# Optimization experiments

Hardware: AMD Instinct MI355X
Metric: run time of the kernel (lower is better)

Reference implementation:

```python
import jax, jax.numpy as jnp
import numpy as np

LATENT = 3
HIDDEN = 16
INP = LATENT + 1  # prev_z cat action
B = 1048576


def setup_inputs() -> dict:
    key = jax.random.key(0)
    ks = jax.random.split(key, 11)
    s_ih = 1.0 / np.sqrt(HIDDEN)
    return {
        "prev_z": jax.random.normal(ks[0], (B, LATENT), jnp.float32),
        "action": jax.random.normal(ks[1], (B, 1), jnp.float32),
        "prev_h": jax.random.normal(ks[2], (B, HIDDEN), jnp.float32),
        # GRUCell params (torch layout: [3*H, in] and [3*H, H], gate order r,z,n)
        "W_ih": jax.random.uniform(ks[3], (3 * HIDDEN, INP), jnp.float32, -s_ih, s_ih),
        "W_hh": jax.random.uniform(ks[4], (3 * HIDDEN, HIDDEN), jnp.float32, -s_ih, s_ih),
        "b_ih": jax.random.uniform(ks[5], (3 * HIDDEN,), jnp.float32, -s_ih, s_ih),
        "b_hh": jax.random.uniform(ks[6], (3 * HIDDEN,), jnp.float32, -s_ih, s_ih),
        # prior heads
        "W_mu": jax.random.uniform(ks[7], (LATENT, HIDDEN), jnp.float32, -s_ih, s_ih),
        "b_mu": jax.random.uniform(ks[8], (LATENT,), jnp.float32, -s_ih, s_ih),
        "W_lv": jax.random.uniform(ks[9], (LATENT, HIDDEN), jnp.float32, -s_ih, s_ih),
        "b_lv": jax.random.uniform(ks[10], (LATENT,), jnp.float32, -s_ih, s_ih),
    }


def reference(prev_z, action, prev_h, W_ih, W_hh, b_ih, b_hh, W_mu, b_mu, W_lv, b_lv):
    x = jnp.concatenate([prev_z, action], axis=-1)              # [B, 4]
    gi = x @ W_ih.T + b_ih                                       # [B, 3H]
    gh = prev_h @ W_hh.T + b_hh                                  # [B, 3H]
    i_r, i_z, i_n = jnp.split(gi, 3, axis=-1)
    h_r, h_z, h_n = jnp.split(gh, 3, axis=-1)
    r = jax.nn.sigmoid(i_r + h_r)
    z = jax.nn.sigmoid(i_z + h_z)
    n = jnp.tanh(i_n + r * h_n)
    h = (1.0 - z) * n + z * prev_h                               # [B, H]
    mu = h @ W_mu.T + b_mu                                       # [B, 3]
    logvar = jnp.clip(h @ W_lv.T + b_lv, -5.0, 5.0)              # [B, 3]
    return mu, logvar, h
```

## Files before the change

### kernel.cpp

```cpp
#include <hip/hip_runtime.h>

#define TPB 256
#define WPT 4

typedef _Float16 half8 __attribute__((ext_vector_type(8)));
typedef float f32x4 __attribute__((ext_vector_type(4)));

__device__ __forceinline__ float fast_sigmoid(float x) {
    return __builtin_amdgcn_rcpf(1.0f + __expf(-x));
}
__device__ __forceinline__ float fast_tanh(float x) {
    return 2.0f * __builtin_amdgcn_rcpf(1.0f + __expf(-2.0f * x)) - 1.0f;
}


__global__ __launch_bounds__(64) void prep_kernel(
    const float* __restrict__ W_ih, const float* __restrict__ W_hh,
    const float* __restrict__ b_ih, const float* __restrict__ b_hh,
    const float* __restrict__ W_mu, const float* __restrict__ b_mu,
    const float* __restrict__ W_lv, const float* __restrict__ b_lv,
    void* __restrict__ wsv)
{
    _Float16* wsB  = (_Float16*)wsv;
    _Float16* wsA2 = wsB + 2048;
    const int l = threadIdx.x;
    const int col = l & 15, kg = l >> 4;

    #pragma unroll
    for (int t = 0; t < 4; ++t) {
        const int gate = (t == 0) ? col : (t == 1) ? (16 + col) : (32 + col);
        #pragma unroll
        for (int i = 0; i < 8; ++i) {
            const int k = kg * 8 + i;
            float v = 0.f;
            if (t <= 1) {
                if (k < 4)       v = W_ih[gate * 4 + k];
                else if (k < 20) v = W_hh[gate * 16 + (k - 4)];
            } else if (t == 2) {
                if (k < 4)       v = W_ih[gate * 4 + k];
            } else {
                if (k >= 4 && k < 20) v = W_hh[gate * 16 + (k - 4)];
            }
            wsB[t * 512 + l * 8 + i] = (_Float16)v;
        }
    }
    #pragma unroll
    for (int i = 0; i < 8; ++i) {
        const int k = kg * 8 + i;
        const int m = col;
        float v = 0.f;
        if (m < 3) {
            if (k < 16)       v = W_mu[m * 16 + k];
            else if (k == 20) v = b_mu[m];
        } else if (m < 6) {
            if (k < 16)       v = W_lv[(m - 3) * 16 + k];
            else if (k == 20) v = b_lv[m - 3];
        }
        wsA2[l * 8 + i] = (_Float16)v;
    }
    if (l < 16) {
        float4* b4 = (float4*)((char*)wsv + 5120);
        b4[l] = make_float4(b_ih[l] + b_hh[l],
                            b_ih[16 + l] + b_hh[16 + l],
                            b_ih[32 + l],
                            b_hh[32 + l]);
    }
}

__global__ __launch_bounds__(TPB) void rssm_kernel(
    const float* __restrict__ prev_z,
    const float* __restrict__ action,
    const float* __restrict__ prev_h,
    const void*  __restrict__ wsv,
    float* __restrict__ out_mu,
    float* __restrict__ out_lv,
    float* __restrict__ out_h,
    int B)
{
    __shared__ float lds[4][WPT][16 * 20];
    const int tid  = threadIdx.x;
    const int wid  = tid >> 6, lane = tid & 63;
    const int col  = lane & 15, kg = lane >> 4;
    const int wbase = (blockIdx.x * 4 + wid) * (16 * WPT);
    if (wbase >= B) return;

    const _Float16* wsB  = (const _Float16*)wsv;
    const _Float16* wsA2 = wsB + 2048;
    const float4*   wsB4 = (const float4*)((const char*)wsv + 5120);

    const half8* Bp = (const half8*)wsB;
    const half8 bR  = Bp[lane];
    const half8 bZ  = Bp[64 + lane];
    const half8 bNi = Bp[128 + lane];
    const half8 bNh = Bp[192 + lane];
    const half8 a2  = ((const half8*)wsA2)[lane];
    const float4 bias = wsB4[col];

    half8 a[WPT];
    if (kg == 0) {
        #pragma unroll
        for (int t = 0; t < WPT; ++t) {
            const int arow = min(wbase + t * 16 + col, B - 1);
            const float z0 = prev_z[arow * 3 + 0];
            const float z1 = prev_z[arow * 3 + 1];
            const float z2 = prev_z[arow * 3 + 2];
            const float ac = action[arow];
            const float4 h03 = *(const float4*)(prev_h + (size_t)arow * 16);
            a[t][0] = (_Float16)z0;    a[t][1] = (_Float16)z1;
            a[t][2] = (_Float16)z2;    a[t][3] = (_Float16)ac;
            a[t][4] = (_Float16)h03.x; a[t][5] = (_Float16)h03.y;
            a[t][6] = (_Float16)h03.z; a[t][7] = (_Float16)h03.w;
        }
    } else if (kg == 1) {
        #pragma unroll
        for (int t = 0; t < WPT; ++t) {
            const int arow = min(wbase + t * 16 + col, B - 1);
            const float4 u = *(const float4*)(prev_h + (size_t)arow * 16 + 4);
            const float4 v = *(const float4*)(prev_h + (size_t)arow * 16 + 8);
            a[t][0] = (_Float16)u.x; a[t][1] = (_Float16)u.y;
            a[t][2] = (_Float16)u.z; a[t][3] = (_Float16)u.w;
            a[t][4] = (_Float16)v.x; a[t][5] = (_Float16)v.y;
            a[t][6] = (_Float16)v.z; a[t][7] = (_Float16)v.w;
        }
    } else if (kg == 2) {
        #pragma unroll
        for (int t = 0; t < WPT; ++t) {
            const int arow = min(wbase + t * 16 + col, B - 1);
            const float4 w = *(const float4*)(prev_h + (size_t)arow * 16 + 12);
            a[t][0] = (_Float16)w.x; a[t][1] = (_Float16)w.y;
            a[t][2] = (_Float16)w.z; a[t][3] = (_Float16)w.w;
            a[t][4] = (_Float16)0.f; a[t][5] = (_Float16)0.f;
            a[t][6] = (_Float16)0.f; a[t][7] = (_Float16)0.f;
        }
    } else {
        #pragma unroll
        for (int t = 0; t < WPT; ++t)
            #pragma unroll
            for (int i = 0; i < 8; ++i) a[t][i] = (_Float16)0.f;
    }

    float hp[WPT][4];
    #pragma unroll
    for (int t = 0; t < WPT; ++t) {
        const int rbase = wbase + t * 16 + kg * 4;
        #pragma unroll
        for (int q = 0; q < 4; ++q)
            hp[t][q] = prev_h[(size_t)min(rbase + q, B - 1) * 16 + col];
    }

    #pragma unroll
    for (int t = 0; t < WPT; ++t) {
        f32x4 accR  = {bias.x, bias.x, bias.x, bias.x};
        f32x4 accZ  = {bias.y, bias.y, bias.y, bias.y};
        f32x4 accNi = {bias.z, bias.z, bias.z, bias.z};
        f32x4 accNh = {bias.w, bias.w, bias.w, bias.w};
        accR  = __builtin_amdgcn_mfma_f32_16x16x32_f16(a[t], bR,  accR,  0, 0, 0);
        accZ  = __builtin_amdgcn_mfma_f32_16x16x32_f16(a[t], bZ,  accZ,  0, 0, 0);
        accNi = __builtin_amdgcn_mfma_f32_16x16x32_f16(a[t], bNi, accNi, 0, 0, 0);
        accNh = __builtin_amdgcn_mfma_f32_16x16x32_f16(a[t], bNh, accNh, 0, 0, 0);

        const int rbase = wbase + t * 16 + kg * 4;
        float* ldst = &lds[wid][t][0];
        #pragma unroll
        for (int q = 0; q < 4; ++q) {
            const float r  = fast_sigmoid(accR[q]);
            const float z  = fast_sigmoid(accZ[q]);
            const float n  = fast_tanh(fmaf(r, accNh[q], accNi[q]));
            const float hv = fmaf(z, hp[t][q] - n, n);
            const int rr = rbase + q;
            if (rr < B) out_h[(size_t)min(rr, B - 1) * 16 + col] = hv;
            ldst[(kg * 4 + q) * 20 + col] = hv;
        }
    }

    #pragma unroll
    for (int t = 0; t < WPT; ++t) {
        half8 b2;
        if (kg < 2) {
            const float4 p0 = *(const float4*)&lds[wid][t][col * 20 + kg * 8];
            const float4 p1 = *(const float4*)&lds[wid][t][col * 20 + kg * 8 + 4];
            b2[0] = (_Float16)p0.x; b2[1] = (_Float16)p0.y;
            b2[2] = (_Float16)p0.z; b2[3] = (_Float16)p0.w;
            b2[4] = (_Float16)p1.x; b2[5] = (_Float16)p1.y;
            b2[6] = (_Float16)p1.z; b2[7] = (_Float16)p1.w;
        } else if (kg == 2) {
            #pragma unroll
            for (int i = 0; i < 8; ++i) b2[i] = (_Float16)0.f;
            b2[4] = (_Float16)1.0f;
        } else {
            #pragma unroll
            for (int i = 0; i < 8; ++i) b2[i] = (_Float16)0.f;
        }

        f32x4 acc2 = {0.f, 0.f, 0.f, 0.f};
        acc2 = __builtin_amdgcn_mfma_f32_16x16x32_f16(a2, b2, acc2, 0, 0, 0);

        const int brow = wbase + t * 16 + col;
        if (brow < B) {
            if (kg == 0) {
                out_mu[brow * 3 + 0] = acc2[0];
                out_mu[brow * 3 + 1] = acc2[1];
                out_mu[brow * 3 + 2] = acc2[2];
                out_lv[brow * 3 + 0] = fminf(fmaxf(acc2[3], -5.0f), 5.0f);
            } else if (kg == 1) {
                out_lv[brow * 3 + 1] = fminf(fmaxf(acc2[0], -5.0f), 5.0f);
                out_lv[brow * 3 + 2] = fminf(fmaxf(acc2[1], -5.0f), 5.0f);
            }
        }
    }
}

extern "C" void kernel_launch(void* const* d_in, const int* in_sizes, int n_in,
                              void* d_out, int out_size, void* d_ws, size_t ws_size,
                              hipStream_t stream) {
    const float* prev_z = (const float*)d_in[0];
    const float* action = (const float*)d_in[1];
    const float* prev_h = (const float*)d_in[2];
    const float* W_ih   = (const float*)d_in[3];
    const float* W_hh   = (const float*)d_in[4];
    const float* b_ih   = (const float*)d_in[5];
    const float* b_hh   = (const float*)d_in[6];
    const float* W_mu   = (const float*)d_in[7];
    const float* b_mu   = (const float*)d_in[8];
    const float* W_lv   = (const float*)d_in[9];
    const float* b_lv   = (const float*)d_in[10];

    const int B = in_sizes[0] / 3;
    float* out    = (float*)d_out;
    float* out_mu = out;
    float* out_lv = out + (size_t)3 * B;
    float* out_h  = out + (size_t)6 * B;

    prep_kernel<<<1, 64, 0, stream>>>(W_ih, W_hh, b_ih, b_hh,
                                      W_mu, b_mu, W_lv, b_lv, d_ws);

    const int rows_per_block = 4 * 16 * WPT;
    const int blocks = (B + rows_per_block - 1) / rows_per_block;
    rssm_kernel<<<blocks, TPB, 0, stream>>>(prev_z, action, prev_h, d_ws,
                                            out_mu, out_lv, out_h, B);
}
```

Baseline: 51.74 us.

## Stage inputs and outputs through LDS for coalesced float4 global access

```diff
diff --git a/kernel.cpp b/kernel.cpp
--- a/kernel.cpp
+++ b/kernel.cpp
@@ -2,8 +2,13 @@
 
 #define TPB 256
 #define WPT 4
+#define ROW_DW 20
+#define LDS_ROW_F32 (64 * ROW_DW)
+#define LDS_MU_F32 192
+#define LDS_WAVE_F32 (LDS_ROW_F32 + 2 * LDS_MU_F32)
 
 typedef _Float16 half8 __attribute__((ext_vector_type(8)));
+typedef __fp16  fp16x2 __attribute__((ext_vector_type(2)));
 typedef float f32x4 __attribute__((ext_vector_type(4)));
 
 __device__ __forceinline__ float fast_sigmoid(float x) {
@@ -11,6 +16,14 @@
 }
 __device__ __forceinline__ float fast_tanh(float x) {
     return 2.0f * __builtin_amdgcn_rcpf(1.0f + __expf(-2.0f * x)) - 1.0f;
+}
+__device__ __forceinline__ half8 pack8(float4 lo, float4 hi) {
+    union { fp16x2 p[4]; half8 h; } u;
+    u.p[0] = __builtin_amdgcn_cvt_pkrtz(lo.x, lo.y);
+    u.p[1] = __builtin_amdgcn_cvt_pkrtz(lo.z, lo.w);
+    u.p[2] = __builtin_amdgcn_cvt_pkrtz(hi.x, hi.y);
+    u.p[3] = __builtin_amdgcn_cvt_pkrtz(hi.z, hi.w);
+    return u.h;
 }
 
 
@@ -21,8 +34,7 @@
     const float* __restrict__ W_lv, const float* __restrict__ b_lv,
     void* __restrict__ wsv)
 {
-    _Float16* wsB  = (_Float16*)wsv;
-    _Float16* wsA2 = wsB + 2048;
+    _Float16* wsB = (_Float16*)wsv;
     const int l = threadIdx.x;
     const int col = l & 15, kg = l >> 4;
 
@@ -47,6 +59,11 @@
     #pragma unroll
     for (int i = 0; i < 8; ++i) {
         const int k = kg * 8 + i;
+        wsB[4 * 512 + l * 8 + i] = (_Float16)((k == col + 4) ? 1.f : 0.f);
+    }
+    #pragma unroll
+    for (int i = 0; i < 8; ++i) {
+        const int k = kg * 8 + i;
         const int m = col;
         float v = 0.f;
         if (m < 3) {
@@ -56,10 +73,10 @@
             if (k < 16)       v = W_lv[(m - 3) * 16 + k];
             else if (k == 20) v = b_lv[m - 3];
         }
-        wsA2[l * 8 + i] = (_Float16)v;
+        wsB[5 * 512 + l * 8 + i] = (_Float16)v;
     }
     if (l < 16) {
-        float4* b4 = (float4*)((char*)wsv + 5120);
+        float4* b4 = (float4*)((char*)wsv + 6144);
         b4[l] = make_float4(b_ih[l] + b_hh[l],
                             b_ih[16 + l] + b_hh[16 + l],
                             b_ih[32 + l],
@@ -77,135 +94,109 @@
     float* __restrict__ out_h,
     int B)
 {
-    __shared__ float lds[4][WPT][16 * 20];
-    const int tid  = threadIdx.x;
-    const int wid  = tid >> 6, lane = tid & 63;
-    const int col  = lane & 15, kg = lane >> 4;
-    const int wbase = (blockIdx.x * 4 + wid) * (16 * WPT);
+    __shared__ float lds[4][LDS_WAVE_F32];
+    const int tid = threadIdx.x;
+    const int wid = tid >> 6, lane = tid & 63;
+    const int col = lane & 15, kg = lane >> 4;
+    const int wbase = (blockIdx.x * 4 + wid) * 64;
     if (wbase >= B) return;
 
-    const _Float16* wsB  = (const _Float16*)wsv;
-    const _Float16* wsA2 = wsB + 2048;
-    const float4*   wsB4 = (const float4*)((const char*)wsv + 5120);
-
-    const half8* Bp = (const half8*)wsB;
+    float* W  = lds[wid];
+    float* MU = W + LDS_ROW_F32;
+    float* LV = MU + LDS_MU_F32;
+
+    const half8* Bp = (const half8*)wsv;
     const half8 bR  = Bp[lane];
     const half8 bZ  = Bp[64 + lane];
     const half8 bNi = Bp[128 + lane];
     const half8 bNh = Bp[192 + lane];
-    const half8 a2  = ((const half8*)wsA2)[lane];
-    const float4 bias = wsB4[col];
-
-    half8 a[WPT];
-    if (kg == 0) {
+    const half8 bHp = Bp[256 + lane];
+    const half8 a2  = Bp[320 + lane];
+    const float4 bias = ((const float4*)((const char*)wsv + 6144))[col];
+
+    {
+        const float4* hg = (const float4*)prev_h;
         #pragma unroll
-        for (int t = 0; t < WPT; ++t) {
-            const int arow = min(wbase + t * 16 + col, B - 1);
-            const float z0 = prev_z[arow * 3 + 0];
-            const float z1 = prev_z[arow * 3 + 1];
-            const float z2 = prev_z[arow * 3 + 2];
-            const float ac = action[arow];
-            const float4 h03 = *(const float4*)(prev_h + (size_t)arow * 16);
-            a[t][0] = (_Float16)z0;    a[t][1] = (_Float16)z1;
-            a[t][2] = (_Float16)z2;    a[t][3] = (_Float16)ac;
-            a[t][4] = (_Float16)h03.x; a[t][5] = (_Float16)h03.y;
-            a[t][6] = (_Float16)h03.z; a[t][7] = (_Float16)h03.w;
-        }
-    } else if (kg == 1) {
-        #pragma unroll
-        for (int t = 0; t < WPT; ++t) {
-            const int arow = min(wbase + t * 16 + col, B - 1);
-            const float4 u = *(const float4*)(prev_h + (size_t)arow * 16 + 4);
-            const float4 v = *(const float4*)(prev_h + (size_t)arow * 16 + 8);
-            a[t][0] = (_Float16)u.x; a[t][1] = (_Float16)u.y;
-            a[t][2] = (_Float16)u.z; a[t][3] = (_Float16)u.w;
-            a[t][4] = (_Float16)v.x; a[t][5] = (_Float16)v.y;
-            a[t][6] = (_Float16)v.z; a[t][7] = (_Float16)v.w;
-        }
-    } else if (kg == 2) {
-        #pragma unroll
-        for (int t = 0; t < WPT; ++t) {
-            const int arow = min(wbase + t * 16 + col, B - 1);
-            const float4 w = *(const float4*)(prev_h + (size_t)arow * 16 + 12);
-            a[t][0] = (_Float16)w.x; a[t][1] = (_Float16)w.y;
-            a[t][2] = (_Float16)w.z; a[t][3] = (_Float16)w.w;
-            a[t][4] = (_Float16)0.f; a[t][5] = (_Float16)0.f;
-            a[t][6] = (_Float16)0.f; a[t][7] = (_Float16)0.f;
-        }
-    } else {
-        #pragma unroll
-        for (int t = 0; t < WPT; ++t)
-            #pragma unroll
-            for (int i = 0; i < 8; ++i) a[t][i] = (_Float16)0.f;
-    }
-
-    float hp[WPT][4];
+        for (int i = 0; i < 4; ++i) {
+            const int fi = i * 64 + lane;
+            const int r = fi >> 2, w = fi & 3;
+            const int gi = min(wbase * 4 + fi, B * 4 - 1);
+            const float4 v = hg[gi];
+            *(float4*)&W[r * ROW_DW + 4 + w * 4] = v;
+        }
+        const int zr = min(wbase + lane, B - 1);
+        const float z0 = prev_z[zr * 3 + 0];
+        const float z1 = prev_z[zr * 3 + 1];
+        const float z2 = prev_z[zr * 3 + 2];
+        const float ac = action[zr];
+        *(float4*)&W[lane * ROW_DW] = make_float4(z0, z1, z2, ac);
+    }
+
     #pragma unroll
     for (int t = 0; t < WPT; ++t) {
-        const int rbase = wbase + t * 16 + kg * 4;
-        #pragma unroll
-        for (int q = 0; q < 4; ++q)
-            hp[t][q] = prev_h[(size_t)min(rbase + q, B - 1) * 16 + col];
-    }
-
-    #pragma unroll
-    for (int t = 0; t < WPT; ++t) {
+        const float* ap = &W[(t * 16 + col) * ROW_DW + kg * 8];
+        const float4 z4 = make_float4(0.f, 0.f, 0.f, 0.f);
+        const float4 p0 = (kg < 3) ? *(const float4*)ap : z4;
+        const float4 p1 = (kg < 2) ? *(const float4*)(ap + 4) : z4;
+        const half8 a = pack8(p0, p1);
+
         f32x4 accR  = {bias.x, bias.x, bias.x, bias.x};
         f32x4 accZ  = {bias.y, bias.y, bias.y, bias.y};
         f32x4 accNi = {bias.z, bias.z, bias.z, bias.z};
         f32x4 accNh = {bias.w, bias.w, bias.w, bias.w};
-        accR  = __builtin_amdgcn_mfma_f32_16x16x32_f16(a[t], bR,  accR,  0, 0, 0);
-        accZ  = __builtin_amdgcn_mfma_f32_16x16x32_f16(a[t], bZ,  accZ,  0, 0, 0);
-        accNi = __builtin_amdgcn_mfma_f32_16x16x32_f16(a[t], bNi, accNi, 0, 0, 0);
-        accNh = __builtin_amdgcn_mfma_f32_16x16x32_f16(a[t], bNh, accNh, 0, 0, 0);
-
-        const int rbase = wbase + t * 16 + kg * 4;
-        float* ldst = &lds[wid][t][0];
+        f32x4 accHp = {0.f, 0.f, 0.f, 0.f};
+        accR  = __builtin_amdgcn_mfma_f32_16x16x32_f16(a, bR,  accR,  0, 0, 0);
+        accZ  = __builtin_amdgcn_mfma_f32_16x16x32_f16(a, bZ,  accZ,  0, 0, 0);
+        accNi = __builtin_amdgcn_mfma_f32_16x16x32_f16(a, bNi, accNi, 0, 0, 0);
+        accNh = __builtin_amdgcn_mfma_f32_16x16x32_f16(a, bNh, accNh, 0, 0, 0);
+        accHp = __builtin_amdgcn_mfma_f32_16x16x32_f16(a, bHp, accHp, 0, 0, 0);
+
         #pragma unroll
         for (int q = 0; q < 4; ++q) {
             const float r  = fast_sigmoid(accR[q]);
             const float z  = fast_sigmoid(accZ[q]);
             const float n  = fast_tanh(fmaf(r, accNh[q], accNi[q]));
-            const float hv = fmaf(z, hp[t][q] - n, n);
-            const int rr = rbase + q;
-            if (rr < B) out_h[(size_t)min(rr, B - 1) * 16 + col] = hv;
-            ldst[(kg * 4 + q) * 20 + col] = hv;
-        }
-    }
-
-    #pragma unroll
-    for (int t = 0; t < WPT; ++t) {
+            const float hv = fmaf(z, accHp[q] - n, n);
+            W[(t * 16 + kg * 4 + q) * ROW_DW + 4 + col] = hv;
+        }
+
         half8 b2;
         if (kg < 2) {
-            const float4 p0 = *(const float4*)&lds[wid][t][col * 20 + kg * 8];
-            const float4 p1 = *(const float4*)&lds[wid][t][col * 20 + kg * 8 + 4];
-            b2[0] = (_Float16)p0.x; b2[1] = (_Float16)p0.y;
-            b2[2] = (_Float16)p0.z; b2[3] = (_Float16)p0.w;
-            b2[4] = (_Float16)p1.x; b2[5] = (_Float16)p1.y;
-            b2[6] = (_Float16)p1.z; b2[7] = (_Float16)p1.w;
-        } else if (kg == 2) {
-            #pragma unroll
-            for (int i = 0; i < 8; ++i) b2[i] = (_Float16)0.f;
-            b2[4] = (_Float16)1.0f;
+            const float* hr = &W[(t * 16 + col) * ROW_DW + 4 + kg * 8];
+            b2 = pack8(*(const float4*)hr, *(const float4*)(hr + 4));
         } else {
             #pragma unroll
             for (int i = 0; i < 8; ++i) b2[i] = (_Float16)0.f;
-        }
-
+            if (kg == 2) b2[4] = (_Float16)1.0f;
+        }
         f32x4 acc2 = {0.f, 0.f, 0.f, 0.f};
         acc2 = __builtin_amdgcn_mfma_f32_16x16x32_f16(a2, b2, acc2, 0, 0, 0);
 
-        const int brow = wbase + t * 16 + col;
-        if (brow < B) {
-            if (kg == 0) {
-                out_mu[brow * 3 + 0] = acc2[0];
-                out_mu[brow * 3 + 1] = acc2[1];
-                out_mu[brow * 3 + 2] = acc2[2];
-                out_lv[brow * 3 + 0] = fminf(fmaxf(acc2[3], -5.0f), 5.0f);
-            } else if (kg == 1) {
-                out_lv[brow * 3 + 1] = fminf(fmaxf(acc2[0], -5.0f), 5.0f);
-                out_lv[brow * 3 + 2] = fminf(fmaxf(acc2[1], -5.0f), 5.0f);
-            }
+        const int mr = (t * 16 + col) * 3;
+        if (kg == 0) {
+            MU[mr + 0] = acc2[0];
+            MU[mr + 1] = acc2[1];
+            MU[mr + 2] = acc2[2];
+            LV[mr + 0] = fminf(fmaxf(acc2[3], -5.0f), 5.0f);
+        } else if (kg == 1) {
+            LV[mr + 1] = fminf(fmaxf(acc2[0], -5.0f), 5.0f);
+            LV[mr + 2] = fminf(fmaxf(acc2[1], -5.0f), 5.0f);
+        }
+
+        {
+            const int r = lane >> 2, w = lane & 3;
+            const float4 hv4 = *(const float4*)&W[(t * 16 + r) * ROW_DW + 4 + w * 4];
+            const int orow = wbase + t * 16 + r;
+            if (orow < B)
+                *(float4*)&out_h[(size_t)orow * 16 + w * 4] = hv4;
+        }
+    }
+
+    if (lane < 48) {
+        const int gi = wbase * 3 + lane * 4;
+        if (gi + 3 < B * 3) {
+            *(float4*)&out_mu[gi] = *(const float4*)&MU[lane * 4];
+            *(float4*)&out_lv[gi] = *(const float4*)&LV[lane * 4];
         }
     }
 }
@@ -234,7 +225,7 @@
     prep_kernel<<<1, 64, 0, stream>>>(W_ih, W_hh, b_ih, b_hh,
                                       W_mu, b_mu, W_lv, b_lv, d_ws);
 
-    const int rows_per_block = 4 * 16 * WPT;
+    const int rows_per_block = 256;
     const int blocks = (B + rows_per_block - 1) / rows_per_block;
     rssm_kernel<<<blocks, TPB, 0, stream>>>(prev_z, action, prev_h, d_ws,
                                             out_mu, out_lv, out_h, B);
```

Result: faster. 42.95 us (-17.0%).
